# Kernel tuning notes

Hardware: AMD Instinct MI355X
Metric: run time of the kernel (lower is better)

Reference implementation:

```python
import jax, jax.numpy as jnp
import numpy as np


def setup_inputs() -> dict:
    key = jax.random.key(0)
    kx, kd = jax.random.split(key)
    B, S, E = 32, 1024, 256
    x = jax.random.normal(kx, (B, S, E), dtype=jnp.float32)
    duration = jax.random.randint(kd, (B, S), 0, 8).astype(jnp.int64)
    return {"x": x, "duration": duration}


def reference(x, duration):
    # x: [B, S, E] float, duration: [B, S] int (mel frames per phoneme)
    B, S, E = x.shape
    cum = jnp.cumsum(duration, axis=1)          # [B, S] exclusive upper boundaries
    mel_len = cum[:, -1]                        # [B]
    max_mel = int(jnp.max(mel_len))             # pad target = batch max (matches torch)
    t = jnp.arange(max_mel)                     # [T]
    # frame t belongs to token i where cum[i-1] <= t < cum[i]; zero-duration
    # tokens are naturally skipped by side='right'.
    idx = jax.vmap(lambda c: jnp.searchsorted(c, t, side='right'))(cum)  # [B, T]
    idx = jnp.minimum(idx, S - 1)
    out = jnp.take_along_axis(x, idx[..., None], axis=1)  # [B, T, E]
    mel_mask = (t[None, :] >= mel_len[:, None]).astype(jnp.int32)  # [B, T], 1 = pad
    out = out * (1 - mel_mask)[..., None].astype(x.dtype)           # zero padded frames
    return out, mel_mask
```

## Files before the change

kernel.cpp:

```cpp
#include <hip/hip_runtime.h>

#define BB 32
#define SS 1024
#define EE 256

typedef float f4 __attribute__((ext_vector_type(4)));

__global__ void lr_cumsum_kernel(const int* __restrict__ dur, int* __restrict__ cum) {
    __shared__ int sdur[SS];
    const int b = blockIdx.x;
    const int lane = threadIdx.x;
    for (int j = lane; j < SS; j += 64) sdur[j] = dur[b * SS + j];
    __syncthreads();

    int vals[16];
    int run = 0;
    const int base = lane * 16;
#pragma unroll
    for (int j = 0; j < 16; ++j) { run += sdur[base + j]; vals[j] = run; }

    int inc = run;
    for (int d = 1; d < 64; d <<= 1) {
        int y = __shfl_up(inc, d, 64);
        if (lane >= d) inc += y;
    }
    const int off = inc - run;
#pragma unroll
    for (int j = 0; j < 16; ++j) cum[b * SS + base + j] = off + vals[j];
}

__global__ void lr_fused_kernel(const float* __restrict__ x,
                                const int* __restrict__ cum,
                                float* __restrict__ out,
                                float* __restrict__ mask,
                                int max_mel) {
    const int b = blockIdx.y;
    const int wave = threadIdx.x >> 6;
    const int lane = threadIdx.x & 63;
    const int t = blockIdx.x * 4 + wave;

    const int* crow = cum + b * SS;
    const int mel_len = crow[SS - 1];
    f4* obase = (f4*)(out + (size_t)b * max_mel * EE);

    if (t < SS) {
        const int c1 = crow[t];
        const int c0 = (t == 0) ? 0 : crow[t - 1];
        if (c1 > c0) {
            const f4* xrow = (const f4*)(x + ((size_t)b * SS + t) * EE);
            const f4 v = __builtin_nontemporal_load(xrow + lane);
            for (int tt = c0; tt < c1; ++tt)
                __builtin_nontemporal_store(v, obase + (size_t)tt * (EE / 4) + lane);
            if (lane == 0)
                for (int tt = c0; tt < c1; ++tt)
                    mask[(size_t)b * max_mel + tt] = 0.0f;
        }
    }
    if (t >= mel_len && t < max_mel) {
        const f4 z = {0.f, 0.f, 0.f, 0.f};
        __builtin_nontemporal_store(z, obase + (size_t)t * (EE / 4) + lane);
        if (lane == 0) mask[(size_t)b * max_mel + t] = 1.0f;
    }
}

extern "C" void kernel_launch(void* const* d_in, const int* in_sizes, int n_in,
                              void* d_out, int out_size, void* d_ws, size_t ws_size,
                              hipStream_t stream) {
    const float* x   = (const float*)d_in[0];
    const int*   dur = (const int*)d_in[1];
    float* out = (float*)d_out;

    const int max_mel = out_size / (BB * (EE + 1));
    float* mask = out + (size_t)BB * max_mel * EE;
    int* cum = (int*)d_ws;

    lr_cumsum_kernel<<<BB, 64, 0, stream>>>(dur, cum);

    const int span = (max_mel > SS) ? max_mel : SS;
    dim3 grid((span + 3) / 4, BB);
    lr_fused_kernel<<<grid, 256, 0, stream>>>(x, cum, out, mask, max_mel);
}
```

Baseline: 148.0 us.

## Switch from token-scatter to per-frame gather via precomputed frame-to-token index

The prep kernel now computes the cumulative sum in shared memory and writes a frame-to-token index map into workspace. The main kernel then assigns one wave per output frame and gathers the matching input row. Before, one wave per token wrote a variable number of frames, which left waves unevenly loaded. The cost is extra index-map writes and reads, plus input rows being re-read once per repeated frame.

```diff
diff --git a/kernel.cpp b/kernel.cpp
--- a/kernel.cpp
+++ b/kernel.cpp
@@ -6,59 +6,69 @@
 
 typedef float f4 __attribute__((ext_vector_type(4)));
 
-__global__ void lr_cumsum_kernel(const int* __restrict__ dur, int* __restrict__ cum) {
+__global__ void lr_prep_kernel(const int* __restrict__ dur,
+                               int* __restrict__ mels,
+                               int* __restrict__ idx,
+                               int max_mel) {
     __shared__ int sdur[SS];
+    __shared__ int scum[SS];
+    __shared__ int stot;
     const int b = blockIdx.x;
-    const int lane = threadIdx.x;
-    for (int j = lane; j < SS; j += 64) sdur[j] = dur[b * SS + j];
+    const int tid = threadIdx.x;
+
+    for (int j = tid; j < SS; j += 256) sdur[j] = dur[b * SS + j];
     __syncthreads();
 
-    int vals[16];
-    int run = 0;
-    const int base = lane * 16;
+    if (tid < 64) {
+        int vals[16];
+        int run = 0;
+        const int base = tid * 16;
 #pragma unroll
-    for (int j = 0; j < 16; ++j) { run += sdur[base + j]; vals[j] = run; }
+        for (int j = 0; j < 16; ++j) { run += sdur[base + j]; vals[j] = run; }
+        int inc = run;
+        for (int d = 1; d < 64; d <<= 1) {
+            int y = __shfl_up(inc, d, 64);
+            if (tid >= d) inc += y;
+        }
+        const int off = inc - run;
+#pragma unroll
+        for (int j = 0; j < 16; ++j) scum[base + j] = off + vals[j];
+        if (tid == 63) stot = inc;
+    }
+    __syncthreads();
 
-    int inc = run;
-    for (int d = 1; d < 64; d <<= 1) {
-        int y = __shfl_up(inc, d, 64);
-        if (lane >= d) inc += y;
+    int* irow = idx + (size_t)b * max_mel;
+    for (int s = tid; s < SS; s += 256) {
+        const int c1 = scum[s];
+        const int c0 = s ? scum[s - 1] : 0;
+        for (int t = c0; t < c1; ++t) irow[t] = s;
     }
-    const int off = inc - run;
-#pragma unroll
-    for (int j = 0; j < 16; ++j) cum[b * SS + base + j] = off + vals[j];
+    if (tid == 0) mels[b] = stot;
 }
 
-__global__ void lr_fused_kernel(const float* __restrict__ x,
-                                const int* __restrict__ cum,
-                                float* __restrict__ out,
-                                float* __restrict__ mask,
-                                int max_mel) {
+__global__ void lr_gather_kernel(const float* __restrict__ x,
+                                 const int* __restrict__ mels,
+                                 const int* __restrict__ idx,
+                                 float* __restrict__ out,
+                                 float* __restrict__ mask,
+                                 int max_mel) {
     const int b = blockIdx.y;
     const int wave = threadIdx.x >> 6;
     const int lane = threadIdx.x & 63;
     const int t = blockIdx.x * 4 + wave;
+    if (t >= max_mel) return;
 
-    const int* crow = cum + b * SS;
-    const int mel_len = crow[SS - 1];
-    f4* obase = (f4*)(out + (size_t)b * max_mel * EE);
+    const int mel_len = mels[b];
+    f4* orow = (f4*)(out + ((size_t)b * max_mel + t) * EE);
 
-    if (t < SS) {
-        const int c1 = crow[t];
-        const int c0 = (t == 0) ? 0 : crow[t - 1];
-        if (c1 > c0) {
-            const f4* xrow = (const f4*)(x + ((size_t)b * SS + t) * EE);
-            const f4 v = __builtin_nontemporal_load(xrow + lane);
-            for (int tt = c0; tt < c1; ++tt)
-                __builtin_nontemporal_store(v, obase + (size_t)tt * (EE / 4) + lane);
-            if (lane == 0)
-                for (int tt = c0; tt < c1; ++tt)
-                    mask[(size_t)b * max_mel + tt] = 0.0f;
-        }
-    }
-    if (t >= mel_len && t < max_mel) {
+    if (t < mel_len) {
+        const int s = idx[(size_t)b * max_mel + t];
+        const f4 v = ((const f4*)(x + ((size_t)b * SS + s) * EE))[lane];
+        __builtin_nontemporal_store(v, orow + lane);
+        if (lane == 0) mask[(size_t)b * max_mel + t] = 0.0f;
+    } else {
         const f4 z = {0.f, 0.f, 0.f, 0.f};
-        __builtin_nontemporal_store(z, obase + (size_t)t * (EE / 4) + lane);
+        __builtin_nontemporal_store(z, orow + lane);
         if (lane == 0) mask[(size_t)b * max_mel + t] = 1.0f;
     }
 }
@@ -72,11 +82,12 @@
 
     const int max_mel = out_size / (BB * (EE + 1));
     float* mask = out + (size_t)BB * max_mel * EE;
-    int* cum = (int*)d_ws;
 
-    lr_cumsum_kernel<<<BB, 64, 0, stream>>>(dur, cum);
+    int* mels = (int*)d_ws;
+    int* idx  = mels + 64;
 
-    const int span = (max_mel > SS) ? max_mel : SS;
-    dim3 grid((span + 3) / 4, BB);
-    lr_fused_kernel<<<grid, 256, 0, stream>>>(x, cum, out, mask, max_mel);
+    lr_prep_kernel<<<BB, 256, 0, stream>>>(dur, mels, idx, max_mel);
+
+    dim3 grid((max_mel + 3) / 4, BB);
+    lr_gather_kernel<<<grid, 256, 0, stream>>>(x, mels, idx, out, mask, max_mel);
 }
```

Result: slower. 163.6 us (+10.5%).

## Fuse cumsum into expand kernel, recomputing per-block prefix sums in shared memory

Applied to the files above, without the earlier changes.

Removes the separate cumsum kernel launch and its global workspace. Each block now loads its batch row of durations (1024 ints) as int4, scans it with wave shuffles plus a cross-wave combine, and keeps the result in shared memory. The mask zero-fill is also parallelised across lanes instead of one lane looping. The cost is that every block redoes the full-row scan, which is redundant work and adds syncthreads latency before the copy starts.

```diff
diff --git a/kernel.cpp b/kernel.cpp
--- a/kernel.cpp
+++ b/kernel.cpp
@@ -5,61 +5,62 @@
 #define EE 256
 
 typedef float f4 __attribute__((ext_vector_type(4)));
+typedef int   i4 __attribute__((ext_vector_type(4)));
 
-__global__ void lr_cumsum_kernel(const int* __restrict__ dur, int* __restrict__ cum) {
-    __shared__ int sdur[SS];
-    const int b = blockIdx.x;
-    const int lane = threadIdx.x;
-    for (int j = lane; j < SS; j += 64) sdur[j] = dur[b * SS + j];
+__global__ void lr_onepass_kernel(const float* __restrict__ x,
+                                  const int* __restrict__ dur,
+                                  float* __restrict__ out,
+                                  float* __restrict__ mask,
+                                  int max_mel) {
+    __shared__ int scum[SS];
+    __shared__ int wtot[4];
+    const int b = blockIdx.y;
+    const int tid = threadIdx.x;
+    const int lane = tid & 63;
+    const int wave = tid >> 6;
+
+    const i4 d = ((const i4*)(dur + b * SS))[tid];
+    const int s0 = d.x;
+    const int s1 = s0 + d.y;
+    const int s2 = s1 + d.z;
+    const int s3 = s2 + d.w;
+    int inc = s3;
+    for (int dd = 1; dd < 64; dd <<= 1) {
+        const int y = __shfl_up(inc, dd, 64);
+        if (lane >= dd) inc += y;
+    }
+    if (lane == 63) wtot[wave] = inc;
+    __syncthreads();
+    int woff = 0;
+#pragma unroll
+    for (int w = 0; w < 4; ++w) woff += (w < wave) ? wtot[w] : 0;
+    const int toff = woff + inc - s3;
+    scum[tid * 4 + 0] = toff + s0;
+    scum[tid * 4 + 1] = toff + s1;
+    scum[tid * 4 + 2] = toff + s2;
+    scum[tid * 4 + 3] = toff + s3;
+    const int mel_len = wtot[0] + wtot[1] + wtot[2] + wtot[3];
     __syncthreads();
 
-    int vals[16];
-    int run = 0;
-    const int base = lane * 16;
-#pragma unroll
-    for (int j = 0; j < 16; ++j) { run += sdur[base + j]; vals[j] = run; }
-
-    int inc = run;
-    for (int d = 1; d < 64; d <<= 1) {
-        int y = __shfl_up(inc, d, 64);
-        if (lane >= d) inc += y;
-    }
-    const int off = inc - run;
-#pragma unroll
-    for (int j = 0; j < 16; ++j) cum[b * SS + base + j] = off + vals[j];
-}
-
-__global__ void lr_fused_kernel(const float* __restrict__ x,
-                                const int* __restrict__ cum,
-                                float* __restrict__ out,
-                                float* __restrict__ mask,
-                                int max_mel) {
-    const int b = blockIdx.y;
-    const int wave = threadIdx.x >> 6;
-    const int lane = threadIdx.x & 63;
     const int t = blockIdx.x * 4 + wave;
-
-    const int* crow = cum + b * SS;
-    const int mel_len = crow[SS - 1];
     f4* obase = (f4*)(out + (size_t)b * max_mel * EE);
+    float* mrow = mask + (size_t)b * max_mel;
 
     if (t < SS) {
-        const int c1 = crow[t];
-        const int c0 = (t == 0) ? 0 : crow[t - 1];
+        const int c1 = scum[t];
+        const int c0 = t ? scum[t - 1] : 0;
         if (c1 > c0) {
             const f4* xrow = (const f4*)(x + ((size_t)b * SS + t) * EE);
             const f4 v = __builtin_nontemporal_load(xrow + lane);
             for (int tt = c0; tt < c1; ++tt)
                 __builtin_nontemporal_store(v, obase + (size_t)tt * (EE / 4) + lane);
-            if (lane == 0)
-                for (int tt = c0; tt < c1; ++tt)
-                    mask[(size_t)b * max_mel + tt] = 0.0f;
+            if (lane < c1 - c0) mrow[c0 + lane] = 0.0f;
         }
     }
     if (t >= mel_len && t < max_mel) {
         const f4 z = {0.f, 0.f, 0.f, 0.f};
         __builtin_nontemporal_store(z, obase + (size_t)t * (EE / 4) + lane);
-        if (lane == 0) mask[(size_t)b * max_mel + t] = 1.0f;
+        if (lane == 0) mrow[t] = 1.0f;
     }
 }
 
@@ -72,11 +73,8 @@
 
     const int max_mel = out_size / (BB * (EE + 1));
     float* mask = out + (size_t)BB * max_mel * EE;
-    int* cum = (int*)d_ws;
-
-    lr_cumsum_kernel<<<BB, 64, 0, stream>>>(dur, cum);
 
     const int span = (max_mel > SS) ? max_mel : SS;
     dim3 grid((span + 3) / 4, BB);
-    lr_fused_kernel<<<grid, 256, 0, stream>>>(x, cum, out, mask, max_mel);
+    lr_onepass_kernel<<<grid, 256, 0, stream>>>(x, dur, out, mask, max_mel);
 }
```

After: 155.6 us. +5.1%, slower.
